# Performance work log

Hardware: AMD Instinct MI355X
Metric: run time of the kernel (lower is better)

## Reference

```python
import jax, jax.numpy as jnp
import numpy as np

D_MODEL = 2048
D_INNER = 4096   # = d_ssm = nheads * headdim
NHEADS = 64      # = ngroups
DSTATE = 64      # = headdim (d_inner == ngroups * d_state)
D_XB = 1024      # GQA-style shared x/B width
XB_HEADS = D_XB // DSTATE    # 16
REP = NHEADS // XB_HEADS     # repeat_group = 4
DCONV = 4
CHUNK = 128
EPS = 1e-5
BATCH, SEQLEN = 1, 4096
D_IN_PROJ = 2 * D_INNER + 2 * D_XB + NHEADS  # d_mlp == 0
CONV_DIM = D_INNER + 2 * D_XB


def setup_inputs() -> dict:
    key = jax.random.key(0)
    ks = jax.random.split(key, 8)
    u = jax.random.normal(ks[0], (BATCH, SEQLEN, D_MODEL), jnp.float32)
    W_in = jax.random.normal(ks[1], (D_MODEL, D_IN_PROJ), jnp.float32) * np.float32(1.0 / np.sqrt(D_MODEL))
    conv_w = jax.random.uniform(ks[2], (CONV_DIM, DCONV), jnp.float32, -0.5, 0.5)
    conv_b = jnp.zeros((CONV_DIM,), jnp.float32)
    # dt_bias = inverse-softplus of dt sampled log-uniform in [dt_min, dt_max]
    dt = jnp.exp(jax.random.uniform(ks[3], (NHEADS,), jnp.float32) * np.float32(np.log(0.1) - np.log(0.001)) + np.float32(np.log(0.001)))
    dt = jnp.clip(dt, 1e-4, None)
    dt_bias = dt + jnp.log(-jnp.expm1(-dt))
    A_log = jnp.log(jax.random.uniform(ks[4], (NHEADS,), jnp.float32, 1.0, 16.0))
    D = jnp.ones((NHEADS,), jnp.float32)
    norm_weight = jnp.ones((D_INNER,), jnp.float32)
    W_out = jax.random.normal(ks[5], (D_INNER, D_MODEL), jnp.float32) * np.float32(1.0 / np.sqrt(D_INNER))
    return {"u": u, "W_in": W_in, "conv_w": conv_w, "conv_b": conv_b,
            "dt_bias": dt_bias, "A_log": A_log, "D": D,
            "norm_weight": norm_weight, "W_out": W_out}


def _ssd_chunked(x, dt, A, Bm, Cm):
    # x: (b,l,h,p), dt: (b,l,h) post-softplus, A: (h,) negative, Bm/Cm: (b,l,h,n)
    b, l, h, p = x.shape
    n = Bm.shape[-1]
    c, q = l // CHUNK, CHUNK
    rs = lambda t: t.reshape(b, c, q, *t.shape[2:])
    x_c, dt_c, B_c, C_c = rs(x), rs(dt), rs(Bm), rs(Cm)
    dA = dt_c * A                       # (b,c,q,h)
    cum = jnp.cumsum(dA, axis=2)        # (b,c,q,h)
    cumT = jnp.moveaxis(cum, 3, 2)      # (b,c,h,q)
    # intra-chunk: y_i += sum_{j<=i} (C_i.B_j) * exp(cum_i - cum_j) * dt_j * x_j
    diff = cumT[..., :, None] - cumT[..., None, :]               # (b,c,h,q,q)
    M = jnp.where(jnp.tril(jnp.ones((q, q), bool)), jnp.exp(diff), 0.0)
    xdt = x_c * dt_c[..., None]                                  # (b,c,q,h,p)
    G = jnp.einsum('bcihn,bcjhn->bchij', C_c, B_c)
    y = jnp.einsum('bchij,bcjhp->bcihp', G * M, xdt)
    # inter-chunk state passing
    decay_to_end = jnp.exp(cum[:, :, -1:, :] - cum)              # (b,c,q,h)
    S = jnp.einsum('bcjhn,bcjh,bcjhp->bchnp', B_c, decay_to_end, xdt)
    chunk_decay = jnp.exp(cum[:, :, -1, :])                      # (b,c,h)

    def step(H, inp):
        S_c, dec = inp
        return dec[..., None, None] * H + S_c, H

    H0 = jnp.zeros((b, h, n, p), x.dtype)
    _, Hprev = jax.lax.scan(step, H0, (jnp.moveaxis(S, 1, 0), jnp.moveaxis(chunk_decay, 1, 0)))
    Hprev = jnp.moveaxis(Hprev, 0, 1)                            # (b,c,h,n,p)
    y = y + jnp.einsum('bcihn,bcih,bchnp->bcihp', C_c, jnp.exp(cum), Hprev)
    return y.reshape(b, l, h, p)


def reference(u, W_in, conv_w, conv_b, dt_bias, A_log, D, norm_weight, W_out):
    b, l, _ = u.shape
    zxbcdt = u @ W_in                                            # (b,l,D_IN_PROJ)
    z = zxbcdt[..., :D_INNER]
    xBC = zxbcdt[..., D_INNER:D_INNER + CONV_DIM]
    dt = zxbcdt[..., D_INNER + CONV_DIM:]
    # depthwise causal conv1d + SiLU (padding d_conv-1 on the left, output len l)
    xp = jnp.pad(xBC, ((0, 0), (DCONV - 1, 0), (0, 0)))
    conv = conv_b + sum(xp[:, k:k + l, :] * conv_w[:, k] for k in range(DCONV))
    xBC = jax.nn.silu(conv)
    x = xBC[..., :D_XB]
    Bc = xBC[..., D_XB:2 * D_XB]
    Cc = xBC[..., 2 * D_XB:]
    # repeat_kv: (b,l,xb_heads,dstate) -> (b,l,nheads,dstate), interleaved repeats
    x = jnp.repeat(x.reshape(b, l, XB_HEADS, DSTATE), REP, axis=2)
    Bm = jnp.repeat(Bc.reshape(b, l, XB_HEADS, DSTATE), REP, axis=2)
    Cm = Cc.reshape(b, l, NHEADS, DSTATE)
    dt = jax.nn.softplus(dt + dt_bias)                           # dt_softplus=True
    A = -jnp.exp(A_log)
    y = _ssd_chunked(x, dt, A, Bm, Cm) + x * D[:, None]          # per-head D skip
    # gated RMSNorm: group size = d_ssm // ngroups = headdim, norm_before_gate=False
    yz = y * jax.nn.silu(z.reshape(b, l, NHEADS, DSTATE))
    normed = yz * jax.lax.rsqrt(jnp.mean(jnp.square(yz), axis=-1, keepdims=True) + EPS)
    out = normed.reshape(b, l, D_INNER) * norm_weight
    return out @ W_out
```

## Files before the change

kernel.cpp:

```cpp
#include <hip/hip_runtime.h>
#include <hip/hip_bf16.h>
#include <math.h>

typedef __hip_bfloat16 bf16;
typedef __attribute__((ext_vector_type(8))) short short8;
typedef __attribute__((ext_vector_type(4))) float f32x4;

#define D_MODEL   2048
#define D_INNER   4096
#define NHEADS    64
#define DSTATE    64
#define D_XB      1024
#define XB_HEADS  16
#define REP       4
#define DCONV     4
#define CHUNK     128
#define SEQLEN    4096
#define NCHUNK    (SEQLEN / CHUNK)
#define D_IN_PROJ (2*D_INNER + 2*D_XB + NHEADS)
#define NPAD      10496
#define CONV_DIM  (D_INNER + 2*D_XB)
#define EPS       1e-5f
#define LOG2E     1.44269504f

#define Z_BYTES    ((size_t)SEQLEN * D_INNER * 2)
#define RAW_BYTES  ((size_t)SEQLEN * CONV_DIM * 2)
#define DTP_BYTES  ((size_t)SEQLEN * NHEADS * 4)
#define CDEC_BYTES ((size_t)NCHUNK * NHEADS * 4)
#define CONV_BYTES ((size_t)SEQLEN * CONV_DIM * 2)
#define S_BYTES    ((size_t)NCHUNK * NHEADS * DSTATE * DSTATE * 4)
#define U_BYTES    ((size_t)SEQLEN * D_MODEL * 2)
#define RREG_BYTES (CONV_BYTES + S_BYTES)
#define WS_BYTES   (Z_BYTES + RAW_BYTES + DTP_BYTES + CDEC_BYTES + RREG_BYTES)

__device__ __forceinline__ short f2bf(float f) {
  bf16 h = __float2bfloat16(f);
  return *reinterpret_cast<short*>(&h);
}
__device__ __forceinline__ float bf2f(short s) {
  unsigned int u = ((unsigned int)(unsigned short)s) << 16;
  union { unsigned int u; float f; } c; c.u = u; return c.f;
}

__device__ __forceinline__ void gload_lds16(const void* g, void* l) {
  typedef __attribute__((address_space(1))) const unsigned int guint;
  typedef __attribute__((address_space(3))) unsigned int luint;
  __builtin_amdgcn_global_load_lds((guint*)g, (luint*)l, 16, 0, 0);
}

__device__ __forceinline__ char* swz128p(char* b, int r, int c) {
  int o = r * 128 + c * 2; o ^= (r & 7) << 4; return b + o;
}
__device__ __forceinline__ const char* swz128p(const char* b, int r, int c) {
  int o = r * 128 + c * 2; o ^= (r & 7) << 4; return b + o;
}
__device__ __forceinline__ char* swz256p(char* b, int r, int c) {
  int o = r * 256 + c * 2; o ^= (r & 15) << 4; return b + o;
}
__device__ __forceinline__ const char* swz256p(const char* b, int r, int c) {
  int o = r * 256 + c * 2; o ^= (r & 15) << 4; return b + o;
}

__global__ void fill_kernel(float* p, size_t n, float v) {
  size_t i = (size_t)blockIdx.x * blockDim.x + threadIdx.x;
  if (i < n) p[i] = v;
}

__global__ __launch_bounds__(256) void cast_f32_bf16(
    const float* __restrict__ in, short* __restrict__ out, size_t n4) {
  size_t i = (size_t)blockIdx.x * 256 + threadIdx.x;
  if (i >= n4) return;
  float4 v = ((const float4*)in)[i];
  short4 o;
  o.x = f2bf(v.x); o.y = f2bf(v.y); o.z = f2bf(v.z); o.w = f2bf(v.w);
  ((short4*)out)[i] = o;
}

__global__ __launch_bounds__(256) void transpose_cast(
    const float* __restrict__ in, short* __restrict__ out, int R, int C) {
  __shared__ float tile[32][130];
  const int r0 = blockIdx.y * 128;
  const int c0 = blockIdx.x * 32;
  const int tid = threadIdx.x;
  {
    int cq = tid & 7;
    int rbase = tid >> 3;
    bool valid = (c0 + cq * 4) < C;
#pragma unroll
    for (int i = 0; i < 4; ++i) {
      int r = rbase + i * 32;
      float4 v = make_float4(0.f, 0.f, 0.f, 0.f);
      if (valid) v = *(const float4*)(in + (size_t)(r0 + r) * C + c0 + cq * 4);
      tile[cq * 4 + 0][r] = v.x;
      tile[cq * 4 + 1][r] = v.y;
      tile[cq * 4 + 2][r] = v.z;
      tile[cq * 4 + 3][r] = v.w;
    }
  }
  __syncthreads();
  {
    int rq = tid & 31;
    int cbase = tid >> 5;
#pragma unroll
    for (int i = 0; i < 4; ++i) {
      int c = cbase + i * 8;
      short4 o;
      o.x = f2bf(tile[c][rq * 4 + 0]);
      o.y = f2bf(tile[c][rq * 4 + 1]);
      o.z = f2bf(tile[c][rq * 4 + 2]);
      o.w = f2bf(tile[c][rq * 4 + 3]);
      *(short4*)(out + (size_t)(c0 + c) * R + r0 + rq * 4) = o;
    }
  }
}


template<int NLOADS, int THREADS>
__device__ __forceinline__ void stage_half(const char* gtile, int rowbytes,
                                           char* ldst, int tid) {
#pragma unroll
  for (int i = 0; i < NLOADS; ++i) {
    int cid = i * THREADS + tid;
    int r = cid >> 2;
    int pos = ((cid & 3) * 16) ^ (((r >> 1) & 3) << 4);
    gload_lds16(gtile + (size_t)r * rowbytes + pos, ldst + cid * 16);
  }
}

__device__ __forceinline__ void bar_only() {
  __builtin_amdgcn_sched_barrier(0);
  __builtin_amdgcn_s_barrier();
  __builtin_amdgcn_sched_barrier(0);
}

template<int N>
__device__ __forceinline__ void wait_bar() {
  __builtin_amdgcn_sched_barrier(0);
  if constexpr (N == 0) asm volatile("s_waitcnt vmcnt(0)" ::: "memory");
  else if constexpr (N == 3) asm volatile("s_waitcnt vmcnt(3)" ::: "memory");
  else if constexpr (N == 4) asm volatile("s_waitcnt vmcnt(4)" ::: "memory");
  __builtin_amdgcn_s_barrier();
  __builtin_amdgcn_sched_barrier(0);
}

template<int BM>
__device__ __forceinline__ void quad_phase(const char* ldsA_kh, const char* ldsB_kh,
    int mh, int wm, int wn, int fr, int kqb, short8 (&b)[4], bool load_b,
    f32x4 (&acc)[BM / 32][4]) {
  constexpr int MF = BM / 64;
  short8 a[MF];
#pragma unroll
  for (int m = 0; m < MF; ++m) {
    int r = wm * (BM / 2) + mh * (BM / 4) + m * 16 + fr;
    a[m] = *(const short8*)(ldsA_kh + r * 64 + (kqb ^ (((r >> 1) & 3) << 4)));
  }
  if (load_b) {
#pragma unroll
    for (int n = 0; n < 4; ++n) {
      int r = wn * 64 + n * 16 + fr;
      b[n] = *(const short8*)(ldsB_kh + r * 64 + (kqb ^ (((r >> 1) & 3) << 4)));
    }
  }
  __builtin_amdgcn_sched_barrier(0);
  __builtin_amdgcn_s_barrier();
  asm volatile("s_waitcnt lgkmcnt(0)" ::: "memory");
  __builtin_amdgcn_sched_barrier(0);
  __builtin_amdgcn_s_setprio(1);
#pragma unroll
  for (int m = 0; m < MF; ++m)
#pragma unroll
    for (int n = 0; n < 4; ++n)
      acc[mh * MF + m][n] = __builtin_amdgcn_mfma_f32_16x16x32_bf16(a[m], b[n], acc[mh * MF + m][n], 0, 0, 0);
  __builtin_amdgcn_s_setprio(0);
}

template<int BM, int BN, int THREADS, int NWN>
__device__ __forceinline__ void gemm_core(const short* A, const short* Bt, int K,
    int rowBase, int colBase, char* lds, f32x4 (&acc)[BM / 32][4]) {
  constexpr int SA = BM * 64;
  constexpr int SB = BN * 64;
  constexpr int NLA = SA / 16 / THREADS;
  constexpr int NLB = SB / 16 / THREADS;
  constexpr int W = NLA + NLB;
  const int tid = threadIdx.x, lane = tid & 63;
  const int w = tid >> 6, wm = w / NWN, wn = w % NWN;
  const int fr = lane & 15, kqb = (lane >> 4) * 16;
  const int NT = K >> 6;
  const int rb = K * 2;
  char* ldsA = lds;
  char* ldsB = lds + 4 * SA;
  const char* Ag = (const char*)(A + (size_t)rowBase * K);
  const char* Bg = (const char*)(Bt + (size_t)colBase * K);
  stage_half<NLA, THREADS>(Ag, rb, ldsA, tid);
  stage_half<NLB, THREADS>(Bg, rb, ldsB, tid);
  stage_half<NLA, THREADS>(Ag + 64, rb, ldsA + SA, tid);
  stage_half<NLB, THREADS>(Bg + 64, rb, ldsB + SB, tid);
  wait_bar<W>();
  for (int t = 0; t < NT; ++t) {
    const int cbA = (t & 1) * 2 * SA, nbA = ((t + 1) & 1) * 2 * SA;
    const int cbB = (t & 1) * 2 * SB, nbB = ((t + 1) & 1) * 2 * SB;
    const size_t ko = (size_t)(t + 1) * 128;
    const bool more = (t + 1 < NT);
    short8 b0[4], b1[4];
    if (more) stage_half<NLA, THREADS>(Ag + ko, rb, ldsA + nbA, tid);
    quad_phase<BM>(ldsA + cbA, ldsB + cbB, 0, wm, wn, fr, kqb, b0, true, acc);
    bar_only();
    if (more) stage_half<NLB, THREADS>(Bg + ko, rb, ldsB + nbB, tid);
    quad_phase<BM>(ldsA + cbA, ldsB + cbB, 1, wm, wn, fr, kqb, b0, false, acc);
    if (more) { wait_bar<W>(); } else { wait_bar<0>(); }
    if (more) stage_half<NLA, THREADS>(Ag + ko + 64, rb, ldsA + nbA + SA, tid);
    quad_phase<BM>(ldsA + cbA + SA, ldsB + cbB + SB, 0, wm, wn, fr, kqb, b1, true, acc);
    bar_only();
    if (more) stage_half<NLB, THREADS>(Bg + ko + 64, rb, ldsB + nbB + SB, tid);
    quad_phase<BM>(ldsA + cbA + SA, ldsB + cbB + SB, 1, wm, wn, fr, kqb, b1, false, acc);
    if (more) { wait_bar<W>(); } else { wait_bar<0>(); }
  }
}

__global__ __launch_bounds__(512) void gemm1_8ph(
    const short* __restrict__ A, const short* __restrict__ Bt,
    bf16* __restrict__ z, bf16* __restrict__ raw, float* __restrict__ dtraw) {
  __shared__ __align__(16) char lds[131072];
  f32x4 acc[8][4] = {};
  const int bid = blockIdx.x;
  const int s = (bid & 7) * 82 + (bid >> 3);
  const int rowBase = (s & 15) * 256;
  const int colBase = (s >> 4) * 256;
  gemm_core<256, 256, 512, 4>(A, Bt, D_MODEL, rowBase, colBase, lds, acc);
  const int lane = threadIdx.x & 63, w = threadIdx.x >> 6;
  const int wm = w >> 2, wn = w & 3;
  const int fr = lane & 15, kq = lane >> 4;
  const int r0 = rowBase + wm * 128 + kq * 4;
  const int c0 = colBase + wn * 64 + fr;
#pragma unroll
  for (int M = 0; M < 8; ++M)
#pragma unroll
    for (int n = 0; n < 4; ++n) {
      int col = c0 + n * 16;
#pragma unroll
      for (int j = 0; j < 4; ++j) {
        int row = r0 + M * 16 + j;
        float v = acc[M][n][j];
        if (col < D_INNER) {
          z[(size_t)row * D_INNER + col] = __float2bfloat16(v);
        } else if (col < D_INNER + CONV_DIM) {
          raw[(size_t)row * CONV_DIM + (col - D_INNER)] = __float2bfloat16(v);
        } else if (col < D_IN_PROJ) {
          dtraw[(size_t)row * NHEADS + (col - D_INNER - CONV_DIM)] = v;
        }
      }
    }
}

__global__ __launch_bounds__(256) void gemm2_8ph(
    const short* __restrict__ A, const short* __restrict__ Bt,
    float* __restrict__ C) {
  __shared__ __align__(16) char lds[65536];
  f32x4 acc[4][4] = {};
  const int bid = blockIdx.x;
  const int s = (bid & 7) * 64 + (bid >> 3);
  const int rowBase = (s & 31) * 128;
  const int colBase = (s >> 5) * 128;
  gemm_core<128, 128, 256, 2>(A, Bt, D_INNER, rowBase, colBase, lds, acc);
  const int lane = threadIdx.x & 63, w = threadIdx.x >> 6;
  const int wm = w >> 1, wn = w & 1;
  const int fr = lane & 15, kq = lane >> 4;
  const int r0 = rowBase + wm * 64 + kq * 4;
  const int c0 = colBase + wn * 64 + fr;
#pragma unroll
  for (int M = 0; M < 4; ++M)
#pragma unroll
    for (int n = 0; n < 4; ++n) {
      int col = c0 + n * 16;
#pragma unroll
      for (int j = 0; j < 4; ++j)
        C[(size_t)(r0 + M * 16 + j) * D_MODEL + col] = acc[M][n][j];
    }
}

__global__ __launch_bounds__(256) void conv_silu_kernel(
    const bf16* __restrict__ raw, const float* __restrict__ cw,
    const float* __restrict__ cb, bf16* __restrict__ convout) {
  int idx = blockIdx.x * 256 + threadIdx.x;
  if (idx >= SEQLEN * (CONV_DIM / 8)) return;
  int t = idx / (CONV_DIM / 8);
  int c8 = (idx % (CONV_DIM / 8)) * 8;
  float acc[8];
  float4 w[8];
#pragma unroll
  for (int q = 0; q < 8; ++q) {
    acc[q] = cb[c8 + q];
    w[q] = ((const float4*)cw)[c8 + q];
  }
#pragma unroll
  for (int k = 0; k < DCONV; ++k) {
    int tt = t - (DCONV - 1) + k;
    if (tt < 0) continue;
    short8 v = *(const short8*)((const short*)raw + (size_t)tt * CONV_DIM + c8);
#pragma unroll
    for (int q = 0; q < 8; ++q)
      acc[q] += bf2f(v[q]) * ((const float*)&w[q])[k];
  }
  short8 o;
#pragma unroll
  for (int q = 0; q < 8; ++q) {
    float s = acc[q] / (1.f + expf(-acc[q]));
    o[q] = f2bf(s);
  }
  *(short8*)((short*)convout + (size_t)t * CONV_DIM + c8) = o;
}

__global__ __launch_bounds__(256) void dt_softplus_kernel(
    float* __restrict__ dtp, const float* __restrict__ dt_bias) {
  int idx = blockIdx.x * blockDim.x + threadIdx.x;
  if (idx >= SEQLEN * NHEADS) return;
  int h = idx & (NHEADS - 1);
  float x = dtp[idx] + dt_bias[h];
  dtp[idx] = (x > 20.f) ? x : log1pf(expf(x));
}

__global__ __launch_bounds__(256) void ssd_passA(
    const bf16* __restrict__ conv, const float* __restrict__ dtp,
    const float* __restrict__ A_log, short* __restrict__ Sbuf,
    float* __restrict__ cdec) {
  __shared__ __align__(16) char sBn[16384];
  __shared__ __align__(16) char sXn[16384];
  __shared__ __align__(16) char sBT[16384];
  __shared__ __align__(16) char sXT[16384];
  __shared__ float sdt[CHUNK], scum2[CHUNK], sw[CHUNK];
  const int chunk = blockIdx.x, h = blockIdx.y, g = h >> 2;
  const int tid = threadIdx.x, lane = tid & 63, wid = tid >> 6;
  const int t0 = chunk * CHUNK;
  const int fr = lane & 15, kq = lane >> 4;
  {
    const short* cg = (const short*)conv;
#pragma unroll
    for (int it = 0; it < 4; ++it) {
      int cid = tid + it * 256;
      int r = cid >> 3, c8 = (cid & 7) * 8;
      size_t rowoff = (size_t)(t0 + r) * CONV_DIM;
      *(short8*)swz128p(sBn, r, c8) = *(const short8*)(cg + rowoff + D_XB + g * 64 + c8);
      *(short8*)swz128p(sXn, r, c8) = *(const short8*)(cg + rowoff + g * 64 + c8);
    }
    if (tid < CHUNK) sdt[tid] = dtp[(size_t)(t0 + tid) * NHEADS + h];
  }
  __syncthreads();
  if (tid < CHUNK) {
    float Ah2 = -expf(A_log[h]) * LOG2E;
    float s_all = 0.f, s_le = 0.f;
    for (int i = 0; i < CHUNK; ++i) {
      float v = sdt[i] * Ah2;
      s_all += v;
      if (i <= tid) s_le += v;
    }
    scum2[tid] = s_le;
    sw[tid] = exp2f(s_all - s_le) * sdt[tid];
    if (tid == 0) cdec[chunk * NHEADS + h] = exp2f(s_all);
  }
  __syncthreads();
  {
    const int col = tid & 63, jb = (tid >> 6) * 32;
#pragma unroll
    for (int it = 0; it < 32; ++it) {
      int j = jb + it;
      *(short*)swz256p(sBT, col, j) = *(const short*)swz128p(sBn, j, col);
      float xv = bf2f(*(const short*)swz128p(sXn, j, col));
      *(short*)swz256p(sXT, col, j) = f2bf(xv * sw[j]);
    }
  }
  __syncthreads();
  f32x4 acc[4] = {};
#pragma unroll
  for (int ks = 0; ks < 4; ++ks) {
    short8 a = *(const short8*)swz256p(sXT, wid * 16 + fr, ks * 32 + kq * 8);
    short8 b[4];
#pragma unroll
    for (int n = 0; n < 4; ++n) b[n] = *(const short8*)swz256p(sBT, n * 16 + fr, ks * 32 + kq * 8);
#pragma unroll
    for (int n = 0; n < 4; ++n)
      acc[n] = __builtin_amdgcn_mfma_f32_16x16x32_bf16(a, b[n], acc[n], 0, 0, 0);
  }
  short* So = Sbuf + ((size_t)(chunk * NHEADS + h)) * (DSTATE * DSTATE);
#pragma unroll
  for (int n = 0; n < 4; ++n)
#pragma unroll
    for (int jj = 0; jj < 4; ++jj) {
      int p = wid * 16 + kq * 4 + jj;
      int nc = n * 16 + fr;
      So[p * 64 + nc] = f2bf(acc[n][jj]);
    }
}

__global__ __launch_bounds__(256) void ssd_passB(
    short* __restrict__ Sbuf, const float* __restrict__ cdec) {
  const int h = blockIdx.x;
  const int base = blockIdx.y * 1024 + threadIdx.x * 4;
  float H[4] = {};
  for (int c = 0; c < NCHUNK; ++c) {
    short4* Sc = (short4*)(Sbuf + ((size_t)(c * NHEADS + h)) * (DSTATE * DSTATE) + base);
    short4 v = *Sc;
    short4 o;
    o.x = f2bf(H[0]); o.y = f2bf(H[1]); o.z = f2bf(H[2]); o.w = f2bf(H[3]);
    *Sc = o;
    float dec = cdec[c * NHEADS + h];
    H[0] = dec * H[0] + bf2f(v.x);
    H[1] = dec * H[1] + bf2f(v.y);
    H[2] = dec * H[2] + bf2f(v.z);
    H[3] = dec * H[3] + bf2f(v.w);
  }
}

__global__ __launch_bounds__(256) void ssd_passC(
    const bf16* __restrict__ z, const bf16* __restrict__ conv,
    const float* __restrict__ dtp, const float* __restrict__ A_log,
    const float* __restrict__ Dv, const float* __restrict__ nw,
    const short* __restrict__ Hprev, bf16* __restrict__ normed) {
  __shared__ __align__(16) char sC[16384];
  __shared__ __align__(16) char sBX[16384];
  __shared__ __align__(16) char sP[32768];
  __shared__ __align__(16) char sST[8192];
  __shared__ float sdt[CHUNK], scum2[CHUNK];
  const int chunk = blockIdx.x, h = blockIdx.y, g = h >> 2;
  const int tid = threadIdx.x, lane = tid & 63, wid = tid >> 6;
  const int t0 = chunk * CHUNK;
  const int fr = lane & 15, kq = lane >> 4;
  const int wi = wid * 32;
  {
    const short* cg = (const short*)conv;
#pragma unroll
    for (int it = 0; it < 4; ++it) {
      int cid = tid + it * 256;
      int r = cid >> 3, c8 = (cid & 7) * 8;
      size_t rowoff = (size_t)(t0 + r) * CONV_DIM;
      *(short8*)swz128p(sC, r, c8) = *(const short8*)(cg + rowoff + 2 * D_XB + h * 64 + c8);
      *(short8*)swz128p(sBX, r, c8) = *(const short8*)(cg + rowoff + D_XB + g * 64 + c8);
      *(short8*)swz128p(sP + 16384, r, c8) = *(const short8*)(cg + rowoff + g * 64 + c8);
    }
    if (tid < CHUNK) sdt[tid] = dtp[(size_t)(t0 + tid) * NHEADS + h];
  }
  __syncthreads();
  if (tid < CHUNK) {
    float Ah2 = -expf(A_log[h]) * LOG2E;
    float s_le = 0.f;
    for (int i = 0; i <= tid; ++i) s_le += sdt[i] * Ah2;
    scum2[tid] = s_le;
  }
  __syncthreads();
  f32x4 accG[2][8] = {};
#pragma unroll
  for (int ks = 0; ks < 2; ++ks) {
    short8 a[2], b[8];
#pragma unroll
    for (int m = 0; m < 2; ++m)
      a[m] = *(const short8*)swz128p(sC, wi + m * 16 + fr, ks * 32 + kq * 8);
#pragma unroll
    for (int n = 0; n < 8; ++n)
      b[n] = *(const short8*)swz128p(sBX, n * 16 + fr, ks * 32 + kq * 8);
#pragma unroll
    for (int m = 0; m < 2; ++m)
#pragma unroll
      for (int n = 0; n < 8; ++n)
        accG[m][n] = __builtin_amdgcn_mfma_f32_16x16x32_bf16(a[m], b[n], accG[m][n], 0, 0, 0);
  }
  __syncthreads();
  {
    const int p = tid & 63, jb = (tid >> 6) * 32;
#pragma unroll
    for (int it = 0; it < 32; ++it) {
      int j = jb + it;
      *(short*)swz256p(sBX, p, j) = *(const short*)swz128p(sP + 16384, j, p);
    }
    const short* Hp = Hprev + ((size_t)(chunk * NHEADS + h)) * (DSTATE * DSTATE);
#pragma unroll
    for (int it = 0; it < 2; ++it) {
      int cid = tid + it * 256;
      int pr = cid >> 3, c8 = (cid & 7) * 8;
      *(short8*)swz128p(sST, pr, c8) = *(const short8*)(Hp + pr * 64 + c8);
    }
  }
  __syncthreads();
#pragma unroll
  for (int m = 0; m < 2; ++m)
#pragma unroll
    for (int jj = 0; jj < 4; ++jj) {
      int i = wi + m * 16 + kq * 4 + jj;
      float ci = scum2[i];
#pragma unroll
      for (int n = 0; n < 8; ++n) {
        int j = n * 16 + fr;
        float w = (j <= i) ? exp2f(ci - scum2[j]) * sdt[j] : 0.f;
        *(short*)swz256p(sP, i, j) = f2bf(accG[m][n][jj] * w);
      }
    }
  __syncthreads();
  f32x4 acc1[2][4] = {};
#pragma unroll
  for (int ks = 0; ks < 4; ++ks) {
    short8 a[2], b[4];
#pragma unroll
    for (int m = 0; m < 2; ++m)
      a[m] = *(const short8*)swz256p(sP, wi + m * 16 + fr, ks * 32 + kq * 8);
#pragma unroll
    for (int n = 0; n < 4; ++n)
      b[n] = *(const short8*)swz256p(sBX, n * 16 + fr, ks * 32 + kq * 8);
#pragma unroll
    for (int m = 0; m < 2; ++m)
#pragma unroll
      for (int n = 0; n < 4; ++n)
        acc1[m][n] = __builtin_amdgcn_mfma_f32_16x16x32_bf16(a[m], b[n], acc1[m][n], 0, 0, 0);
  }
  f32x4 acc2[2][4] = {};
#pragma unroll
  for (int ks = 0; ks < 2; ++ks) {
    short8 a[2], b[4];
#pragma unroll
    for (int m = 0; m < 2; ++m)
      a[m] = *(const short8*)swz128p(sC, wi + m * 16 + fr, ks * 32 + kq * 8);
#pragma unroll
    for (int n = 0; n < 4; ++n)
      b[n] = *(const short8*)swz128p(sST, n * 16 + fr, ks * 32 + kq * 8);
#pragma unroll
    for (int m = 0; m < 2; ++m)
#pragma unroll
      for (int n = 0; n < 4; ++n)
        acc2[m][n] = __builtin_amdgcn_mfma_f32_16x16x32_bf16(a[m], b[n], acc2[m][n], 0, 0, 0);
  }
  const float Dh = Dv[h];
#pragma unroll
  for (int m = 0; m < 2; ++m)
#pragma unroll
    for (int jj = 0; jj < 4; ++jj) {
      int i = wi + m * 16 + kq * 4 + jj;
      int t = t0 + i;
      float e2 = exp2f(scum2[i]);
      float vs[4];
      float ss = 0.f;
#pragma unroll
      for (int n = 0; n < 4; ++n) {
        int p = n * 16 + fr;
        float xv = bf2f(((const short*)conv)[(size_t)t * CONV_DIM + g * 64 + p]);
        float zv = bf2f(((const short*)z)[(size_t)t * D_INNER + h * 64 + p]);
        float y = acc1[m][n][jj] + e2 * acc2[m][n][jj] + xv * Dh;
        float sz = zv / (1.f + expf(-zv));
        float v = y * sz;
        vs[n] = v;
        ss += v * v;
      }
      ss += __shfl_xor(ss, 1);
      ss += __shfl_xor(ss, 2);
      ss += __shfl_xor(ss, 4);
      ss += __shfl_xor(ss, 8);
      float rinv = rsqrtf(ss * (1.f / 64.f) + EPS);
#pragma unroll
      for (int n = 0; n < 4; ++n) {
        int p = n * 16 + fr;
        ((short*)normed)[(size_t)t * D_INNER + h * 64 + p] = f2bf(vs[n] * rinv * nw[h * 64 + p]);
      }
    }
}

extern "C" void kernel_launch(void* const* d_in, const int* in_sizes, int n_in,
                              void* d_out, int out_size, void* d_ws, size_t ws_size,
                              hipStream_t stream) {
  const float* u       = (const float*)d_in[0];
  const float* W_in    = (const float*)d_in[1];
  const float* conv_w  = (const float*)d_in[2];
  const float* conv_b  = (const float*)d_in[3];
  const float* dt_bias = (const float*)d_in[4];
  const float* A_log   = (const float*)d_in[5];
  const float* Dv      = (const float*)d_in[6];
  const float* norm_w  = (const float*)d_in[7];
  const float* W_out   = (const float*)d_in[8];
  float* out = (float*)d_out;

  if (ws_size < WS_BYTES) {
    size_t n = (size_t)out_size;
    fill_kernel<<<(n + 255) / 256, 256, 0, stream>>>(out, n, 1000.0f);
    return;
  }

  char* wsb   = (char*)d_ws;
  bf16*  z    = (bf16*)(wsb);
  bf16*  raw  = (bf16*)(wsb + Z_BYTES);
  float* dtp  = (float*)(wsb + Z_BYTES + RAW_BYTES);
  float* cdec = (float*)(wsb + Z_BYTES + RAW_BYTES + DTP_BYTES);
  char*  R    = wsb + Z_BYTES + RAW_BYTES + DTP_BYTES + CDEC_BYTES;
  short* u_bf  = (short*)(R);
  short* WinT  = (short*)(R + U_BYTES);
  bf16*  conv  = (bf16*)(R);
  short* Sbuf  = (short*)(R + CONV_BYTES);
  short* WoutT = (short*)(R);
  bf16*  normed = raw;

  cast_f32_bf16<<<(U_BYTES / 8 + 255) / 256, 256, 0, stream>>>(u, u_bf, U_BYTES / 8);
  {
    dim3 grid(NPAD / 32, D_MODEL / 128);
    transpose_cast<<<grid, 256, 0, stream>>>(W_in, WinT, D_MODEL, D_IN_PROJ);
  }
  gemm1_8ph<<<(NPAD / 256) * (SEQLEN / 256), 512, 0, stream>>>(u_bf, WinT, z, raw, dtp);
  conv_silu_kernel<<<(SEQLEN * (CONV_DIM / 8) + 255) / 256, 256, 0, stream>>>(raw, conv_w, conv_b, conv);
  dt_softplus_kernel<<<(SEQLEN * NHEADS + 255) / 256, 256, 0, stream>>>(dtp, dt_bias);
  {
    dim3 grid(NCHUNK, NHEADS);
    ssd_passA<<<grid, 256, 0, stream>>>(conv, dtp, A_log, Sbuf, cdec);
  }
  {
    dim3 grid(NHEADS, 4);
    ssd_passB<<<grid, 256, 0, stream>>>(Sbuf, cdec);
  }
  {
    dim3 grid(NCHUNK, NHEADS);
    ssd_passC<<<grid, 256, 0, stream>>>(z, conv, dtp, A_log, Dv, norm_w, Sbuf, normed);
  }
  {
    dim3 grid(D_MODEL / 32, D_INNER / 128);
    transpose_cast<<<grid, 256, 0, stream>>>(W_out, WoutT, D_INNER, D_MODEL);
  }
  gemm2_8ph<<<(SEQLEN / 128) * (D_MODEL / 128), 256, 0, stream>>>((const short*)normed, WoutT, out);
}
```

Before: 551.6 us.

## Fuse B/C conv+SiLU into SSD passes, only precompute x channel

The standalone conv+SiLU kernel now only produces the x slice (D_XB channels). The B and C channels are computed on the fly inside ssd_passA and ssd_passC from the raw projection output, and the normed buffer is moved so raw stays intact. This removes the write and re-read of most of the conv output. In exchange, B is recomputed by every head in a group (4x redundancy) in both passes, which adds extra raw reads and exp work inside the SSD kernels.

```diff
diff --git a/kernel.cpp b/kernel.cpp
--- a/kernel.cpp
+++ b/kernel.cpp
@@ -59,6 +59,33 @@
 }
 __device__ __forceinline__ const char* swz256p(const char* b, int r, int c) {
   int o = r * 256 + c * 2; o ^= (r & 15) << 4; return b + o;
+}
+
+__device__ __forceinline__ short8 conv8(const short* raw, int t, int ch,
+                                        const float* cw, const float* cb) {
+  float a[8];
+  float4 w[8];
+#pragma unroll
+  for (int q = 0; q < 8; ++q) {
+    a[q] = cb[ch + q];
+    w[q] = ((const float4*)cw)[ch + q];
+  }
+#pragma unroll
+  for (int k = 0; k < DCONV; ++k) {
+    int tt = t - (DCONV - 1) + k;
+    if (tt < 0) continue;
+    short8 v = *(const short8*)(raw + (size_t)tt * CONV_DIM + ch);
+#pragma unroll
+    for (int q = 0; q < 8; ++q)
+      a[q] += bf2f(v[q]) * ((const float*)&w[q])[k];
+  }
+  short8 o;
+#pragma unroll
+  for (int q = 0; q < 8; ++q) {
+    float s = a[q] / (1.f + expf(-a[q]));
+    o[q] = f2bf(s);
+  }
+  return o;
 }
 
 __global__ void fill_kernel(float* p, size_t n, float v) {
@@ -278,36 +305,15 @@
     }
 }
 
-__global__ __launch_bounds__(256) void conv_silu_kernel(
+__global__ __launch_bounds__(256) void conv_silu_x(
     const bf16* __restrict__ raw, const float* __restrict__ cw,
-    const float* __restrict__ cb, bf16* __restrict__ convout) {
+    const float* __restrict__ cb, bf16* __restrict__ convx) {
   int idx = blockIdx.x * 256 + threadIdx.x;
-  if (idx >= SEQLEN * (CONV_DIM / 8)) return;
-  int t = idx / (CONV_DIM / 8);
-  int c8 = (idx % (CONV_DIM / 8)) * 8;
-  float acc[8];
-  float4 w[8];
-#pragma unroll
-  for (int q = 0; q < 8; ++q) {
-    acc[q] = cb[c8 + q];
-    w[q] = ((const float4*)cw)[c8 + q];
-  }
-#pragma unroll
-  for (int k = 0; k < DCONV; ++k) {
-    int tt = t - (DCONV - 1) + k;
-    if (tt < 0) continue;
-    short8 v = *(const short8*)((const short*)raw + (size_t)tt * CONV_DIM + c8);
-#pragma unroll
-    for (int q = 0; q < 8; ++q)
-      acc[q] += bf2f(v[q]) * ((const float*)&w[q])[k];
-  }
-  short8 o;
-#pragma unroll
-  for (int q = 0; q < 8; ++q) {
-    float s = acc[q] / (1.f + expf(-acc[q]));
-    o[q] = f2bf(s);
-  }
-  *(short8*)((short*)convout + (size_t)t * CONV_DIM + c8) = o;
+  if (idx >= SEQLEN * (D_XB / 8)) return;
+  int t = idx / (D_XB / 8);
+  int c8 = (idx % (D_XB / 8)) * 8;
+  short8 o = conv8((const short*)raw, t, c8, cw, cb);
+  *(short8*)((short*)convx + (size_t)t * D_XB + c8) = o;
 }
 
 __global__ __launch_bounds__(256) void dt_softplus_kernel(
@@ -320,9 +326,10 @@
 }
 
 __global__ __launch_bounds__(256) void ssd_passA(
-    const bf16* __restrict__ conv, const float* __restrict__ dtp,
-    const float* __restrict__ A_log, short* __restrict__ Sbuf,
-    float* __restrict__ cdec) {
+    const bf16* __restrict__ raw, const bf16* __restrict__ convx,
+    const float* __restrict__ cw, const float* __restrict__ cb,
+    const float* __restrict__ dtp, const float* __restrict__ A_log,
+    short* __restrict__ Sbuf, float* __restrict__ cdec) {
   __shared__ __align__(16) char sBn[16384];
   __shared__ __align__(16) char sXn[16384];
   __shared__ __align__(16) char sBT[16384];
@@ -333,14 +340,15 @@
   const int t0 = chunk * CHUNK;
   const int fr = lane & 15, kq = lane >> 4;
   {
-    const short* cg = (const short*)conv;
+    const short* cx = (const short*)convx;
 #pragma unroll
     for (int it = 0; it < 4; ++it) {
       int cid = tid + it * 256;
       int r = cid >> 3, c8 = (cid & 7) * 8;
-      size_t rowoff = (size_t)(t0 + r) * CONV_DIM;
-      *(short8*)swz128p(sBn, r, c8) = *(const short8*)(cg + rowoff + D_XB + g * 64 + c8);
-      *(short8*)swz128p(sXn, r, c8) = *(const short8*)(cg + rowoff + g * 64 + c8);
+      *(short8*)swz128p(sBn, r, c8) =
+          conv8((const short*)raw, t0 + r, D_XB + g * 64 + c8, cw, cb);
+      *(short8*)swz128p(sXn, r, c8) =
+          *(const short8*)(cx + (size_t)(t0 + r) * D_XB + g * 64 + c8);
     }
     if (tid < CHUNK) sdt[tid] = dtp[(size_t)(t0 + tid) * NHEADS + h];
   }
@@ -411,10 +419,12 @@
 }
 
 __global__ __launch_bounds__(256) void ssd_passC(
-    const bf16* __restrict__ z, const bf16* __restrict__ conv,
-    const float* __restrict__ dtp, const float* __restrict__ A_log,
-    const float* __restrict__ Dv, const float* __restrict__ nw,
-    const short* __restrict__ Hprev, bf16* __restrict__ normed) {
+    const bf16* __restrict__ z, const bf16* __restrict__ raw,
+    const bf16* __restrict__ convx, const float* __restrict__ cw,
+    const float* __restrict__ cb, const float* __restrict__ dtp,
+    const float* __restrict__ A_log, const float* __restrict__ Dv,
+    const float* __restrict__ nw, const short* __restrict__ Hprev,
+    bf16* __restrict__ normed) {
   __shared__ __align__(16) char sC[16384];
   __shared__ __align__(16) char sBX[16384];
   __shared__ __align__(16) char sP[32768];
@@ -426,15 +436,17 @@
   const int fr = lane & 15, kq = lane >> 4;
   const int wi = wid * 32;
   {
-    const short* cg = (const short*)conv;
+    const short* cx = (const short*)convx;
 #pragma unroll
     for (int it = 0; it < 4; ++it) {
       int cid = tid + it * 256;
       int r = cid >> 3, c8 = (cid & 7) * 8;
-      size_t rowoff = (size_t)(t0 + r) * CONV_DIM;
-      *(short8*)swz128p(sC, r, c8) = *(const short8*)(cg + rowoff + 2 * D_XB + h * 64 + c8);
-      *(short8*)swz128p(sBX, r, c8) = *(const short8*)(cg + rowoff + D_XB + g * 64 + c8);
-      *(short8*)swz128p(sP + 16384, r, c8) = *(const short8*)(cg + rowoff + g * 64 + c8);
+      *(short8*)swz128p(sC, r, c8) =
+          conv8((const short*)raw, t0 + r, 2 * D_XB + h * 64 + c8, cw, cb);
+      *(short8*)swz128p(sBX, r, c8) =
+          conv8((const short*)raw, t0 + r, D_XB + g * 64 + c8, cw, cb);
+      *(short8*)swz128p(sP + 16384, r, c8) =
+          *(const short8*)(cx + (size_t)(t0 + r) * D_XB + g * 64 + c8);
     }
     if (tid < CHUNK) sdt[tid] = dtp[(size_t)(t0 + tid) * NHEADS + h];
   }
@@ -526,6 +538,7 @@
         acc2[m][n] = __builtin_amdgcn_mfma_f32_16x16x32_bf16(a[m], b[n], acc2[m][n], 0, 0, 0);
   }
   const float Dh = Dv[h];
+  const short* cx = (const short*)convx;
 #pragma unroll
   for (int m = 0; m < 2; ++m)
 #pragma unroll
@@ -538,7 +551,7 @@
 #pragma unroll
       for (int n = 0; n < 4; ++n) {
         int p = n * 16 + fr;
-        float xv = bf2f(((const short*)conv)[(size_t)t * CONV_DIM + g * 64 + p]);
+        float xv = bf2f(cx[(size_t)t * D_XB + g * 64 + p]);
         float zv = bf2f(((const short*)z)[(size_t)t * D_INNER + h * 64 + p]);
         float y = acc1[m][n][jj] + e2 * acc2[m][n][jj] + xv * Dh;
         float sz = zv / (1.f + expf(-zv));
@@ -587,10 +600,10 @@
   char*  R    = wsb + Z_BYTES + RAW_BYTES + DTP_BYTES + CDEC_BYTES;
   short* u_bf  = (short*)(R);
   short* WinT  = (short*)(R + U_BYTES);
-  bf16*  conv  = (bf16*)(R);
+  bf16*  convx = (bf16*)(R);
+  bf16*  normed = (bf16*)(R + U_BYTES);
   short* Sbuf  = (short*)(R + CONV_BYTES);
   short* WoutT = (short*)(R);
-  bf16*  normed = raw;
 
   cast_f32_bf16<<<(U_BYTES / 8 + 255) / 256, 256, 0, stream>>>(u, u_bf, U_BYTES / 8);
   {
@@ -598,11 +611,11 @@
     transpose_cast<<<grid, 256, 0, stream>>>(W_in, WinT, D_MODEL, D_IN_PROJ);
   }
   gemm1_8ph<<<(NPAD / 256) * (SEQLEN / 256), 512, 0, stream>>>(u_bf, WinT, z, raw, dtp);
-  conv_silu_kernel<<<(SEQLEN * (CONV_DIM / 8) + 255) / 256, 256, 0, stream>>>(raw, conv_w, conv_b, conv);
+  conv_silu_x<<<(SEQLEN * (D_XB / 8) + 255) / 256, 256, 0, stream>>>(raw, conv_w, conv_b, convx);
   dt_softplus_kernel<<<(SEQLEN * NHEADS + 255) / 256, 256, 0, stream>>>(dtp, dt_bias);
   {
     dim3 grid(NCHUNK, NHEADS);
-    ssd_passA<<<grid, 256, 0, stream>>>(conv, dtp, A_log, Sbuf, cdec);
+    ssd_passA<<<grid, 256, 0, stream>>>(raw, convx, conv_w, conv_b, dtp, A_log, Sbuf, cdec);
   }
   {
     dim3 grid(NHEADS, 4);
@@ -610,7 +623,7 @@
   }
   {
     dim3 grid(NCHUNK, NHEADS);
-    ssd_passC<<<grid, 256, 0, stream>>>(z, conv, dtp, A_log, Dv, norm_w, Sbuf, normed);
+    ssd_passC<<<grid, 256, 0, stream>>>(z, raw, convx, conv_w, conv_b, dtp, A_log, Dv, norm_w, Sbuf, normed);
   }
   {
     dim3 grid(D_MODEL / 32, D_INNER / 128);
```

New measurement: 591.0 us. 7.1% more time.
